# Kernel optimization log

Hardware: AMD Instinct MI355X
Metric: run time of the kernel (lower is better)

## Reference

```python
import jax, jax.numpy as jnp
import numpy as np

BUFF = 10  # buff_size from __init__


def setup_inputs() -> dict:
    key = jax.random.key(0)
    k1, k2, k3, k4 = jax.random.split(key, 4)
    B, N, H, W = 8, 4096, 2048, 2048
    scores = jax.random.uniform(k1, (B, N), dtype=jnp.float32)
    # points in [-1, 1) as the module expects ((points+1)/2 maps into image coords)
    points = jax.random.uniform(k2, (B, N, 2), dtype=jnp.float32, minval=-1.0, maxval=1.0)
    gt_segment = jax.random.randint(k3, (B, 1, H, W), 0, 2, dtype=jnp.int32)
    ps_segments = jax.random.randint(k4, (B, H, W), 0, 2, dtype=jnp.int32)
    return {"scores": scores, "points": points, "gt_segment": gt_segment, "ps_segments": ps_segments}


def reference(scores, points, gt_segment, ps_segments):
    B, _, H, W = gt_segment.shape
    # --- no_grad block in the original ---
    p = jax.lax.stop_gradient((points + 1.0) / 2.0)
    px = (p[:, :, 0] * W).astype(jnp.int32)  # [B,N]
    py = (p[:, :, 1] * H).astype(jnp.int32)
    tx = jnp.clip(px - BUFF, 0, W - 1)
    ty = jnp.clip(py - BUFF, 0, H - 1)
    bx = jnp.clip(px + BUFF, 0, W - 1)
    by = jnp.clip(py + BUFF, 0, H - 1)
    # equality mask and 2D integral image (zero-padded on top/left)
    mask = (gt_segment[:, 0] == ps_segments).astype(jnp.float32)  # [B,H,W]
    S = jnp.pad(jnp.cumsum(jnp.cumsum(mask, axis=1), axis=2), ((0, 0), (1, 0), (1, 0)))  # [B,H+1,W+1]
    bi = jnp.arange(B)[:, None]  # [B,1] batch index
    # sum of mask over half-open window [ty:by, tx:bx) for each point
    cnt = S[bi, by, bx] - S[bi, ty, bx] - S[bi, by, tx] + S[bi, ty, tx]  # [B,N]
    area = ((tx - bx) * (ty - by)).astype(jnp.float32)  # (neg)*(neg) = window area
    scores_gt = jnp.clip(jnp.abs(cnt / area), 0.0, 1.0)
    # --- MSE loss ---
    loss = jnp.mean((scores - scores_gt) ** 2)
    return (loss, scores_gt)
```

## Files before the change

### kernel.cpp

```cpp
#include <hip/hip_runtime.h>

#define BUFF 10

constexpr int B = 8, N = 4096, H = 2048, W = 2048;
constexpr int WAVES_PER_BLOCK = 4;
constexpr int NBLOCKS = (B * N) / WAVES_PER_BLOCK;
constexpr int KW = 21;
constexpr int KCELLS = KW * KW;
constexpr int KITER = (KCELLS + 63) / 64;

__global__ __launch_bounds__(256) void score_windows(
    const float* __restrict__ scores, const float* __restrict__ points,
    const int* __restrict__ gt, const int* __restrict__ ps,
    float* __restrict__ out, float* __restrict__ partial)
{
    const int tid  = blockIdx.x * blockDim.x + threadIdx.x;
    const int idx  = tid >> 6;
    const int lane = threadIdx.x & 63;
    const int wid  = threadIdx.x >> 6;

    const int b = idx >> 12;

    const float vx = points[2 * idx + 0];
    const float vy = points[2 * idx + 1];
    const int px = (int)(((vx + 1.0f) / 2.0f) * (float)W);
    const int py = (int)(((vy + 1.0f) / 2.0f) * (float)H);

    const int tx = min(max(px - BUFF, 0), W - 1);
    const int ty = min(max(py - BUFF, 0), H - 1);
    const int bx = min(max(px + BUFF, 0), W - 1);
    const int by = min(max(py + BUFF, 0), H - 1);

    const int ww = bx - tx;
    const int hh = by - ty;
    const int total = ww * hh;

    const int* __restrict__ gtb = gt + (size_t)b * (size_t)(H * W);
    const int* __restrict__ psb = ps + (size_t)b * (size_t)(H * W);

    int acc = 0;
    #pragma unroll
    for (int k = 0; k < KITER; ++k) {
        const int i = lane + k * 64;
        const int r = i / KW;
        const int c = i - r * KW;
        const bool valid = (i < KCELLS) & (r < hh) & (c < ww);
        const int rr = min(r, hh - 1);
        const int cc = min(c, ww - 1);
        const int off = (ty + rr) * W + (tx + cc);
        const int g = gtb[off];
        const int p = psb[off];
        acc += (valid && (g == p)) ? 1 : 0;
    }

    #pragma unroll
    for (int o = 32; o > 0; o >>= 1) acc += __shfl_down(acc, o, 64);

    __shared__ float wsum[WAVES_PER_BLOCK];
    if (lane == 0) {
        const float sgt = fminf(fmaxf(fabsf((float)acc / (float)total), 0.0f), 1.0f);
        out[1 + idx] = sgt;
        const float d = scores[idx] - sgt;
        wsum[wid] = d * d;
    }
    __syncthreads();
    if (threadIdx.x == 0) {
        partial[blockIdx.x] = wsum[0] + wsum[1] + wsum[2] + wsum[3];
    }
}

__global__ __launch_bounds__(1024) void loss_reduce(
    const float* __restrict__ partial, float* __restrict__ out, int nparts)
{
    __shared__ float sdata[1024];
    float s = 0.0f;
    for (int i = threadIdx.x; i < nparts; i += 1024) s += partial[i];
    sdata[threadIdx.x] = s;
    __syncthreads();
    #pragma unroll
    for (int k = 512; k > 0; k >>= 1) {
        if (threadIdx.x < k) sdata[threadIdx.x] += sdata[threadIdx.x + k];
        __syncthreads();
    }
    if (threadIdx.x == 0) out[0] = sdata[0] / (float)(B * N);
}

extern "C" void kernel_launch(void* const* d_in, const int* in_sizes, int n_in,
                              void* d_out, int out_size, void* d_ws, size_t ws_size,
                              hipStream_t stream) {
    const float* scores = (const float*)d_in[0];
    const float* points = (const float*)d_in[1];
    const int*   gt     = (const int*)d_in[2];
    const int*   ps     = (const int*)d_in[3];
    float* out     = (float*)d_out;
    float* partial = (float*)d_ws;

    score_windows<<<NBLOCKS, 256, 0, stream>>>(scores, points, gt, ps, out, partial);
    loss_reduce<<<1, 1024, 0, stream>>>(partial, out, NBLOCKS);
}
```

Measured before the change: 44.93 us.

## Bin points by batch and row band so nearby windows share an XCD L2

Adds a binning pass that bucket-sorts points by batch and 128-row band using atomic counters, with a fixed capacity per bucket. The scoring kernel then walks buckets, mapping each bucket to one XCD through the block index, so that overlapping window rows are reused in that XCD's L2 instead of being fetched at random across the device. The loss is now computed by a single block that reads the written scores, rather than from per-block partial sums. This adds a memset, an extra launch and a serial single-block reduction over all points. Any points beyond a bucket's capacity would be silently dropped.

```diff
diff --git a/kernel.cpp b/kernel.cpp
--- a/kernel.cpp
+++ b/kernel.cpp
@@ -3,41 +3,34 @@
 #define BUFF 10
 
 constexpr int B = 8, N = 4096, H = 2048, W = 2048;
-constexpr int WAVES_PER_BLOCK = 4;
-constexpr int NBLOCKS = (B * N) / WAVES_PER_BLOCK;
+constexpr int NPTS = B * N;
 constexpr int KW = 21;
 constexpr int KCELLS = KW * KW;
 constexpr int KITER = (KCELLS + 63) / 64;
 
-__global__ __launch_bounds__(256) void score_windows(
-    const float* __restrict__ scores, const float* __restrict__ points,
-    const int* __restrict__ gt, const int* __restrict__ ps,
-    float* __restrict__ out, float* __restrict__ partial)
-{
-    const int tid  = blockIdx.x * blockDim.x + threadIdx.x;
-    const int idx  = tid >> 6;
-    const int lane = threadIdx.x & 63;
-    const int wid  = threadIdx.x >> 6;
+constexpr int NBUCK = 128;
+constexpr int CAP = 512;
+constexpr int PTS_PER_BLOCK = 4;
+constexpr int GRPS = CAP / PTS_PER_BLOCK;
+constexpr size_t WS_NEEDED = 512 + (size_t)NBUCK * CAP * 4;
 
-    const int b = idx >> 12;
-
-    const float vx = points[2 * idx + 0];
-    const float vy = points[2 * idx + 1];
+__device__ __forceinline__ void window_of_point(const float* __restrict__ pts, int idx,
+                                                int& tx, int& ty, int& ww, int& hh, int& total) {
+    const float vx = pts[2 * idx + 0];
+    const float vy = pts[2 * idx + 1];
     const int px = (int)(((vx + 1.0f) / 2.0f) * (float)W);
     const int py = (int)(((vy + 1.0f) / 2.0f) * (float)H);
-
-    const int tx = min(max(px - BUFF, 0), W - 1);
-    const int ty = min(max(py - BUFF, 0), H - 1);
+    tx = min(max(px - BUFF, 0), W - 1);
+    ty = min(max(py - BUFF, 0), H - 1);
     const int bx = min(max(px + BUFF, 0), W - 1);
     const int by = min(max(py + BUFF, 0), H - 1);
+    ww = bx - tx;
+    hh = by - ty;
+    total = ww * hh;
+}
 
-    const int ww = bx - tx;
-    const int hh = by - ty;
-    const int total = ww * hh;
-
-    const int* __restrict__ gtb = gt + (size_t)b * (size_t)(H * W);
-    const int* __restrict__ psb = ps + (size_t)b * (size_t)(H * W);
-
+__device__ __forceinline__ float gather_score(const int* __restrict__ gtb, const int* __restrict__ psb,
+                                              int tx, int ty, int ww, int hh, int total, int lane) {
     int acc = 0;
     #pragma unroll
     for (int k = 0; k < KITER; ++k) {
@@ -52,29 +45,62 @@
         const int p = psb[off];
         acc += (valid && (g == p)) ? 1 : 0;
     }
-
     #pragma unroll
     for (int o = 32; o > 0; o >>= 1) acc += __shfl_down(acc, o, 64);
-
-    __shared__ float wsum[WAVES_PER_BLOCK];
-    if (lane == 0) {
-        const float sgt = fminf(fmaxf(fabsf((float)acc / (float)total), 0.0f), 1.0f);
-        out[1 + idx] = sgt;
-        const float d = scores[idx] - sgt;
-        wsum[wid] = d * d;
-    }
-    __syncthreads();
-    if (threadIdx.x == 0) {
-        partial[blockIdx.x] = wsum[0] + wsum[1] + wsum[2] + wsum[3];
-    }
+    return fminf(fmaxf(fabsf((float)acc / (float)total), 0.0f), 1.0f);
 }
 
-__global__ __launch_bounds__(1024) void loss_reduce(
-    const float* __restrict__ partial, float* __restrict__ out, int nparts)
+
+__global__ __launch_bounds__(256) void bin_points(const float* __restrict__ pts,
+                                                  int* __restrict__ cnt, int* __restrict__ slots) {
+    const int idx = blockIdx.x * 256 + threadIdx.x;
+    if (idx >= NPTS) return;
+    const int b = idx >> 12;
+    const float vy = pts[2 * idx + 1];
+    int py = (int)(((vy + 1.0f) / 2.0f) * (float)H);
+    py = min(max(py, 0), H - 1);
+    const int key = (b << 4) | (py >> 7);
+    const int pos = atomicAdd(&cnt[key], 1);
+    if (pos < CAP) slots[key * CAP + pos] = idx;
+}
+
+__global__ __launch_bounds__(256) void score_windows_binned(
+    const float* __restrict__ pts, const int* __restrict__ gt, const int* __restrict__ ps,
+    const int* __restrict__ cnt, const int* __restrict__ slots, float* __restrict__ out)
 {
+    const int bid = blockIdx.x;
+    const int xcd = bid & 7;
+    const int t = bid >> 3;
+    const int slot_grp = t & (GRPS - 1);
+    const int bwx = t >> 7;
+    const int bucket = bwx * 8 + xcd;
+
+    const int wid = threadIdx.x >> 6;
+    const int lane = threadIdx.x & 63;
+    const int slot = slot_grp * PTS_PER_BLOCK + wid;
+
+    const int nc = min(cnt[bucket], CAP);
+    if (slot >= nc) return;
+    const int idx = slots[bucket * CAP + slot];
+
+    int tx, ty, ww, hh, total;
+    window_of_point(pts, idx, tx, ty, ww, hh, total);
+    const int b = idx >> 12;
+    const int* __restrict__ gtb = gt + (size_t)b * (size_t)(H * W);
+    const int* __restrict__ psb = ps + (size_t)b * (size_t)(H * W);
+
+    const float sgt = gather_score(gtb, psb, tx, ty, ww, hh, total, lane);
+    if (lane == 0) out[1 + idx] = sgt;
+}
+
+__global__ __launch_bounds__(1024) void loss_from_scores(const float* __restrict__ scores,
+                                                         float* __restrict__ out) {
     __shared__ float sdata[1024];
     float s = 0.0f;
-    for (int i = threadIdx.x; i < nparts; i += 1024) s += partial[i];
+    for (int i = threadIdx.x; i < NPTS; i += 1024) {
+        const float d = scores[i] - out[1 + i];
+        s += d * d;
+    }
     sdata[threadIdx.x] = s;
     __syncthreads();
     #pragma unroll
@@ -82,7 +108,24 @@
         if (threadIdx.x < k) sdata[threadIdx.x] += sdata[threadIdx.x + k];
         __syncthreads();
     }
-    if (threadIdx.x == 0) out[0] = sdata[0] / (float)(B * N);
+    if (threadIdx.x == 0) out[0] = sdata[0] / (float)NPTS;
+}
+
+
+__global__ __launch_bounds__(256) void score_windows_flat(
+    const float* __restrict__ pts, const int* __restrict__ gt, const int* __restrict__ ps,
+    float* __restrict__ out)
+{
+    const int tid = blockIdx.x * blockDim.x + threadIdx.x;
+    const int idx = tid >> 6;
+    const int lane = threadIdx.x & 63;
+    int tx, ty, ww, hh, total;
+    window_of_point(pts, idx, tx, ty, ww, hh, total);
+    const int b = idx >> 12;
+    const int* __restrict__ gtb = gt + (size_t)b * (size_t)(H * W);
+    const int* __restrict__ psb = ps + (size_t)b * (size_t)(H * W);
+    const float sgt = gather_score(gtb, psb, tx, ty, ww, hh, total, lane);
+    if (lane == 0) out[1 + idx] = sgt;
 }
 
 extern "C" void kernel_launch(void* const* d_in, const int* in_sizes, int n_in,
@@ -92,9 +135,16 @@
     const float* points = (const float*)d_in[1];
     const int*   gt     = (const int*)d_in[2];
     const int*   ps     = (const int*)d_in[3];
-    float* out     = (float*)d_out;
-    float* partial = (float*)d_ws;
+    float* out = (float*)d_out;
 
-    score_windows<<<NBLOCKS, 256, 0, stream>>>(scores, points, gt, ps, out, partial);
-    loss_reduce<<<1, 1024, 0, stream>>>(partial, out, NBLOCKS);
+    if (ws_size >= WS_NEEDED) {
+        int* cnt   = (int*)d_ws;
+        int* slots = (int*)((char*)d_ws + 512);
+        hipMemsetAsync(cnt, 0, 512, stream);
+        bin_points<<<(NPTS + 255) / 256, 256, 0, stream>>>(points, cnt, slots);
+        score_windows_binned<<<NBUCK * GRPS, 256, 0, stream>>>(points, gt, ps, cnt, slots, out);
+    } else {
+        score_windows_flat<<<NPTS / PTS_PER_BLOCK, 256, 0, stream>>>(points, gt, ps, out);
+    }
+    loss_from_scores<<<1, 1024, 0, stream>>>(scores, out);
 }
```

After: 67.20 us. 1.5x slower.
